# Performance work log

Measured on AMD Instinct MI355X. Metric: run time of the kernel, lower is better.

## Reference

```python
import jax, jax.numpy as jnp
from jax import lax
import numpy as np

K = 10            # size_feat
N_MU = 10         # number of mean-PSF components
NCH = K * K + N_MU  # 110 depthwise channels
KLEN = 65         # precomputed kernel length


def setup_inputs() -> dict:
    key = jax.random.key(0)
    ks = jax.random.split(key, 12)
    B, C, H, W = 1, 3, 256, 256
    img = jax.random.uniform(ks[0], (B, C, H, W), jnp.float32)
    zernike = jax.random.normal(ks[1], (B, H, W, 35), jnp.float32)
    # pos displacements (first 2 channels) scaled to a few pixels
    zernike = zernike.at[..., :2].multiply(2.0)
    fc1_w = jax.random.normal(ks[2], (200, 33), jnp.float32) / np.float32(np.sqrt(33))
    fc1_b = jax.random.normal(ks[3], (200,), jnp.float32) * 0.01
    fc2_w = jax.random.normal(ks[4], (200, 200), jnp.float32) / np.float32(np.sqrt(200))
    fc2_b = jax.random.normal(ks[5], (200,), jnp.float32) * 0.01
    fc3_w = jax.random.normal(ks[6], (100, 200), jnp.float32) * 0.01
    fc3_b = jnp.zeros((100,), jnp.float32)
    basis_left = jax.random.normal(ks[7], (KLEN, K), jnp.float32) * 0.05
    basis_right = jax.random.normal(ks[8], (KLEN, K), jnp.float32) * 0.05
    mu = jax.random.uniform(ks[9], (KLEN, N_MU), jnp.float32) / np.float32(KLEN)
    return dict(img=img, zernike=zernike, fc1_w=fc1_w, fc1_b=fc1_b,
                fc2_w=fc2_w, fc2_b=fc2_b, fc3_w=fc3_w, fc3_b=fc3_b,
                basis_left=basis_left, basis_right=basis_right, mu=mu, ksize=65)


def _grid_sample_border(img, pos):
    """Bilinear grid_sample, padding_mode='border', align_corners=False.
    img: (B,C,H,W), pos: (B,H,W,2) pixel displacements (x,y)."""
    B, C, H, W = img.shape
    yy, xx = jnp.meshgrid(jnp.arange(H, dtype=jnp.float32),
                          jnp.arange(W, dtype=jnp.float32), indexing='ij')
    grid = jnp.stack((xx, yy), -1)                       # (H,W,2)
    wh = jnp.array([W - 1, H - 1], jnp.float32)
    flow = 2.0 * (grid[None] + pos) / wh - 1.0           # (B,H,W,2) in [-1,1]
    ix = ((flow[..., 0] + 1.0) * W - 1.0) * 0.5
    iy = ((flow[..., 1] + 1.0) * H - 1.0) * 0.5
    ix = jnp.clip(ix, 0.0, W - 1)
    iy = jnp.clip(iy, 0.0, H - 1)
    x0 = jnp.floor(ix); y0 = jnp.floor(iy)
    wx = ix - x0;       wy = iy - y0
    x0i = jnp.clip(x0.astype(jnp.int32), 0, W - 1)
    y0i = jnp.clip(y0.astype(jnp.int32), 0, H - 1)
    x1i = jnp.clip(x0i + 1, 0, W - 1)
    y1i = jnp.clip(y0i + 1, 0, H - 1)

    def bilerp(im, x0i, x1i, y0i, y1i, wx, wy):
        g = lambda yi, xi: im[:, yi, xi]                 # (C,H,W)
        top = g(y0i, x0i) * (1 - wx) + g(y0i, x1i) * wx
        bot = g(y1i, x0i) * (1 - wx) + g(y1i, x1i) * wx
        return top * (1 - wy) + bot * wy

    return jax.vmap(bilerp)(img, x0i, x1i, y0i, y1i, wx, wy)


def _depthwise(x, w, pad_axis, pad):
    # x: (N, NCH, H, W); w: (NCH,1,kh,kw). Reflect 'same' padding on pad_axis.
    cfg = [(0, 0)] * 4
    cfg[pad_axis] = (pad, pad)
    xp = jnp.pad(x, cfg, mode='reflect')
    return lax.conv_general_dilated(
        xp, w, (1, 1), 'VALID',
        dimension_numbers=('NCHW', 'OIHW', 'NCHW'),
        feature_group_count=x.shape[1])


def _forward(img, zernike, fc1_w, fc1_b, fc2_w, fc2_b, fc3_w, fc3_b,
             basis_left, basis_right, mu, ksize):
    B, C, H, W = img.shape
    pad = ksize // 2
    # --- grid-sample warp ---
    tilt = _grid_sample_border(img, zernike[..., :2])    # (B,C,H,W)
    # --- per-pixel MLP -> PSF coefficients ---
    f = zernike[..., 2:]                                  # (B,H,W,33)
    h = jax.nn.leaky_relu(f @ fc1_w.T + fc1_b)
    h = jax.nn.leaky_relu(h @ fc2_w.T + fc2_b)
    coef = h @ fc3_w.T + fc3_b                            # (B,H,W,100)
    weight = jnp.concatenate(
        [coef, jnp.ones((B, H, W, N_MU), coef.dtype)], -1)  # (B,H,W,110)
    # --- elementwise weight multiply ---
    big = jnp.concatenate([tilt, jnp.ones_like(tilt)], 1)  # (B,2C,H,W)
    big = big[..., None] * weight[:, None]                 # (B,2C,H,W,110)
    x = big.reshape(B * 2 * C, H, W, NCH).transpose(0, 3, 1, 2)  # (B*2C,110,H,W)
    # --- separable depthwise blur kernels (outer products Z_i x X_j + mu) ---
    wl = jnp.concatenate([jnp.repeat(basis_left.T, K, axis=0), mu.T], 0)  # (110,klen)
    wr = jnp.concatenate([jnp.tile(basis_right.T, (K, 1)), mu.T], 0)      # (110,klen)
    wl = wl[:, None, :, None]                              # (110,1,klen,1)
    wr = wr[:, None, None, :]                              # (110,1,1,klen)
    y = _depthwise(x, wl, 2, pad)
    y = _depthwise(y, wr, 3, pad)
    d = y.reshape(B, 2 * C, NCH, H, W)
    out = jnp.sum(d[:, :3], axis=2) / jnp.sum(d[:, 3:], axis=2)  # (B,3,H,W)
    return out


def reference(img, zernike, fc1_w, fc1_b, fc2_w, fc2_b, fc3_w, fc3_b,
              basis_left, basis_right, mu, ksize):
    return _forward(img, zernike, fc1_w, fc1_b, fc2_w, fc2_b, fc3_w, fc3_b,
                    basis_left, basis_right, mu, ksize)
```

## Files before the change

kernel.cpp:

```cpp
#include <hip/hip_runtime.h>

#define HW 65536

typedef __attribute__((ext_vector_type(8))) short short8;
typedef __attribute__((ext_vector_type(4))) float float4v;

__device__ __forceinline__ int refl(int i){ if (i < 0) i = -i; if (i > 255) i = 510 - i; return i; }
__device__ __forceinline__ float lrelu(float x){ return x > 0.f ? x : 0.01f * x; }
__device__ __forceinline__ unsigned int f2bf(float x){
  union { float f; unsigned int u; } v; v.f = x;
  unsigned int r = v.u + 0x7fff + ((v.u >> 16) & 1);
  return r >> 16;
}
__device__ __forceinline__ unsigned int pk_bf16(float lo, float hi){
  unsigned int r;
  asm("v_cvt_pk_bf16_f32 %0, %1, %2" : "=v"(r) : "v"(lo), "v"(hi));
  return r;
}
__device__ __forceinline__ unsigned short f2h(float x){
  union { _Float16 h; unsigned short u; } v; v.h = (_Float16)x; return v.u;
}
__device__ __forceinline__ float h2f(unsigned short u){
  union { _Float16 h; unsigned short u; } v; v.u = u; return (float)v.h;
}

#define W2OFF 13312
#define W3OFF 59904
__global__ __launch_bounds__(256) void k_prep(const float* __restrict__ img,
    const float* __restrict__ zern,
    const float* __restrict__ w1, const float* __restrict__ w2,
    const float* __restrict__ w3, const float* __restrict__ bl,
    const float* __restrict__ br, const float* __restrict__ mu,
    unsigned short* __restrict__ wbf, unsigned short* __restrict__ Tt,
    float* __restrict__ mucp, float* __restrict__ tilt){
  __shared__ float sm[650];
  __shared__ float sq[10];
  int bid = blockIdx.x;
  int tid = threadIdx.x;
  if (bid < 512){
    int i = bid * 256 + tid;
    if (i < 84992){
      if (i < 208 * 64){
        int n = i >> 6, k = i & 63;
        float v = (n < 200 && k < 33) ? w1[n * 33 + k] : 0.f;
        wbf[i] = (unsigned short)f2bf(v);
      } else if (i < W2OFF + 208 * 224){
        int j = i - W2OFF; int n = j / 224, k = j - n * 224;
        float v = (n < 200 && k < 200) ? w2[n * 200 + k] : 0.f;
        wbf[i] = (unsigned short)f2bf(v);
      } else {
        int j = i - W3OFF; int n = j / 224, k = j - n * 224;
        float v = (n < 100 && k < 200) ? w3[n * 200 + k] : 0.f;
        wbf[i] = (unsigned short)f2bf(v);
      }
    } else {
      int e = i - 84992;
      int t = e / 1536, rem = e - t * 1536;
      int m = rem / 96, k = rem - m * 96;
      int d = k - m;
      float v = 0.f;
      if (d >= 0 && d <= 64){
        if (t < 10)      v = bl[d * 10 + t];
        else if (t < 20) v = mu[d * 10 + (t - 10)];
        else             v = br[d * 10 + (t - 20)];
      }
      Tt[e] = (unsigned short)f2bf(v);
    }
  } else if (bid == 512){
    for (int e = tid; e < 650; e += 256) sm[e] = mu[e];
    __syncthreads();
    if (tid < 10){
      float s = 0.f;
      for (int u = 0; u < 65; ++u) s += sm[u * 10 + tid];
      sq[tid] = s * s;
    }
    __syncthreads();
    if (tid == 0){
      float m = 0.f;
      #pragma unroll
      for (int mm = 0; mm < 10; ++mm) m += sq[mm];
      mucp[0] = m;
    }
  } else {
    int x = tid, y = bid - 513;
    int pix = y * 256 + x;
    float px = zern[pix * 35 + 0], py = zern[pix * 35 + 1];
    float ix = ((float)x + px) * (256.f / 255.f) - 0.5f;
    float iy = ((float)y + py) * (256.f / 255.f) - 0.5f;
    ix = fminf(fmaxf(ix, 0.f), 255.f);
    iy = fminf(fmaxf(iy, 0.f), 255.f);
    float x0f = floorf(ix), y0f = floorf(iy);
    float wx = ix - x0f, wy = iy - y0f;
    int x0 = (int)x0f, y0 = (int)y0f;
    int x1 = min(x0 + 1, 255), y1 = min(y0 + 1, 255);
    #pragma unroll
    for (int c = 0; c < 3; ++c){
      const float* im = img + c * HW;
      float g00 = im[y0 * 256 + x0], g01 = im[y0 * 256 + x1];
      float g10 = im[y1 * 256 + x0], g11 = im[y1 * 256 + x1];
      float top = g00 * (1.f - wx) + g01 * wx;
      float bot = g10 * (1.f - wx) + g11 * wx;
      tilt[c * HW + pix] = top * (1.f - wy) + bot * wy;
    }
  }
}

#define HSTR 232
#define BUFB 14848
__global__ __launch_bounds__(512) void k_mlp(const float* __restrict__ zern,
    const float* __restrict__ b1f, const float* __restrict__ b2f,
    const float* __restrict__ b3f, const unsigned short* __restrict__ wbf,
    unsigned short* __restrict__ coefb){
  __shared__ char smem[2 * BUFB];
  unsigned short* H1  = (unsigned short*)smem;
  unsigned short* XB  = (unsigned short*)(smem + BUFB);
  unsigned short* H2  = XB;
  int tid = threadIdx.x;
  int pix0 = blockIdx.x * 32;
  int lane = tid & 63, wv = tid >> 6;
  int ln = lane & 15, qd = lane >> 4;

  for (int e = tid; e < 1152; e += 512) ((int*)XB)[e] = 0;
  for (int e = tid; e < 384; e += 512){
    int m = e / 12, j = e - m * 12;
    ((int*)H1)[m * 116 + 104 + j] = 0;
  }
  __syncthreads();
  for (int e = tid; e < 32 * 33; e += 512){
    int m = e / 33, k = e - m * 33;
    XB[m * 72 + k] = (unsigned short)f2bf(zern[(pix0 + m) * 35 + 2 + k]);
  }
  __syncthreads();

  for (int nt = wv; nt < 13; nt += 8){
    int n = nt * 16 + ln;
    short8 b0 = *(const short8*)(wbf + n * 64 + qd * 8);
    short8 b1 = *(const short8*)(wbf + n * 64 + 32 + qd * 8);
    float bv = (n < 200) ? b1f[n] : 0.f;
    #pragma unroll
    for (int mt = 0; mt < 2; ++mt){
      float4v acc = {bv, bv, bv, bv};
      short8 a0 = *(const short8*)(XB + (mt * 16 + ln) * 72 + qd * 8);
      short8 a1 = *(const short8*)(XB + (mt * 16 + ln) * 72 + 32 + qd * 8);
      acc = __builtin_amdgcn_mfma_f32_16x16x32_bf16(a0, b0, acc, 0, 0, 0);
      acc = __builtin_amdgcn_mfma_f32_16x16x32_bf16(a1, b1, acc, 0, 0, 0);
      #pragma unroll
      for (int r = 0; r < 4; ++r)
        H1[(mt * 16 + qd * 4 + r) * HSTR + n] = (unsigned short)f2bf(lrelu(acc[r]));
    }
  }
  __syncthreads();

  for (int e = tid; e < 384; e += 512){
    int m = e / 12, j = e - m * 12;
    ((int*)H2)[m * 116 + 104 + j] = 0;
  }
  {
    const unsigned short* w2p = wbf + W2OFF;
    for (int nt = wv; nt < 13; nt += 8){
      int n = nt * 16 + ln;
      short8 bf[7];
      #pragma unroll
      for (int kc = 0; kc < 7; ++kc)
        bf[kc] = *(const short8*)(w2p + n * 224 + kc * 32 + qd * 8);
      float bv = (n < 200) ? b2f[n] : 0.f;
      #pragma unroll
      for (int mt = 0; mt < 2; ++mt){
        float4v acc = {bv, bv, bv, bv};
        #pragma unroll
        for (int kc = 0; kc < 7; ++kc){
          short8 af = *(const short8*)(H1 + (mt * 16 + ln) * HSTR + kc * 32 + qd * 8);
          acc = __builtin_amdgcn_mfma_f32_16x16x32_bf16(af, bf[kc], acc, 0, 0, 0);
        }
        #pragma unroll
        for (int r = 0; r < 4; ++r)
          H2[(mt * 16 + qd * 4 + r) * HSTR + n] = (unsigned short)f2bf(lrelu(acc[r]));
      }
    }
  }
  __syncthreads();

  {
    const unsigned short* w3p = wbf + W3OFF;
    for (int nt = wv; nt < 7; nt += 8){
      int n = nt * 16 + ln;
      short8 bf[7];
      #pragma unroll
      for (int kc = 0; kc < 7; ++kc)
        bf[kc] = *(const short8*)(w3p + n * 224 + kc * 32 + qd * 8);
      float bv = (n < 100) ? b3f[n] : 0.f;
      #pragma unroll
      for (int mt = 0; mt < 2; ++mt){
        float4v acc = {bv, bv, bv, bv};
        #pragma unroll
        for (int kc = 0; kc < 7; ++kc){
          short8 af = *(const short8*)(H2 + (mt * 16 + ln) * HSTR + kc * 32 + qd * 8);
          acc = __builtin_amdgcn_mfma_f32_16x16x32_bf16(af, bf[kc], acc, 0, 0, 0);
        }
        if (n < 100){
          unsigned int lo = (unsigned int)f2h(acc[0]) | ((unsigned int)f2h(acc[1]) << 16);
          unsigned int hi = (unsigned int)f2h(acc[2]) | ((unsigned int)f2h(acc[3]) << 16);
          uint2 val; val.x = lo; val.y = hi;
          *(uint2*)(coefb + n * HW + pix0 + mt * 16 + qd * 4) = val;
        }
      }
    }
  }
}

#define VB 344
__global__ __launch_bounds__(256) void k_vconv16(const float* __restrict__ tilt,
    const unsigned short* __restrict__ coefb, const unsigned short* __restrict__ Tt,
    unsigned short* __restrict__ sbuf, unsigned short* __restrict__ smu){
  __shared__ __align__(16) unsigned short sxb[2][16 * VB];
  int tid = threadIdx.x;
  int bid = blockIdx.x;
  int lane = tid & 63, wv = tid >> 6;
  int ln = lane & 15, qd = lane >> 4;
  int col = tid & 15, seg = tid >> 4;
  int r0 = seg * 20;

  int goff[20];
  #pragma unroll
  for (int q = 0; q < 20; ++q) goff[q] = refl(r0 + q - 32) * 256 + col;

  for (int e = tid; e < 768; e += 256){
    int b = e / 384, r = e - b * 384;
    int cc = r / 24, rp = r - cc * 24;
    sxb[b][cc * VB + 320 + rp] = 0;
  }

  if (bid < 640){
    int s = bid & 15;
    int cj = bid >> 4;
    int c = cj / 10, j = cj - c * 10;
    int x0 = s * 16;
    float treg[20];
    if (c < 3){
      const float* tc = tilt + c * HW + x0;
      #pragma unroll
      for (int q = 0; q < 20; ++q) treg[q] = tc[goff[q]];
    }
    unsigned short pf[20];
    {
      const unsigned short* cq = coefb + j * HW + x0;
      #pragma unroll
      for (int q = 0; q < 20; ++q) pf[q] = cq[goff[q]];
    }
    float4v acc[4];
    #pragma unroll
    for (int t = 0; t < 4; ++t) acc[t] = (float4v){0.f, 0.f, 0.f, 0.f};
    for (int i = 0; i < 10; ++i){
      int us = i & 1;
      unsigned short* sb = sxb[us];
      if (c < 3){
        #pragma unroll
        for (int q = 0; q < 10; ++q){
          float v0 = h2f(pf[2 * q]) * treg[2 * q];
          float v1 = h2f(pf[2 * q + 1]) * treg[2 * q + 1];
          *(unsigned int*)&sb[col * VB + r0 + 2 * q] = pk_bf16(v0, v1);
        }
      } else {
        #pragma unroll
        for (int q = 0; q < 10; ++q){
          *(unsigned int*)&sb[col * VB + r0 + 2 * q] = pk_bf16(h2f(pf[2 * q]), h2f(pf[2 * q + 1]));
        }
      }
      __syncthreads();
      if (i < 9){
        const unsigned short* cn = coefb + ((i + 1) * 10 + j) * HW + x0;
        #pragma unroll
        for (int q = 0; q < 20; ++q) pf[q] = cn[goff[q]];
      }
      const unsigned short* ta = Tt + i * 1536 + ln * 96 + qd * 8;
      short8 A0 = *(const short8*)(ta);
      short8 A1 = *(const short8*)(ta + 32);
      short8 A2 = *(const short8*)(ta + 64);
      #pragma unroll
      for (int t = 0; t < 4; ++t){
        int yt = wv * 4 + t;
        const unsigned short* bp = sb + ln * VB + yt * 16 + qd * 8;
        short8 B0 = *(const short8*)(bp);
        short8 B1 = *(const short8*)(bp + 32);
        short8 B2 = *(const short8*)(bp + 64);
        acc[t] = __builtin_amdgcn_mfma_f32_16x16x32_bf16(A0, B0, acc[t], 0, 0, 0);
        acc[t] = __builtin_amdgcn_mfma_f32_16x16x32_bf16(A1, B1, acc[t], 0, 0, 0);
        acc[t] = __builtin_amdgcn_mfma_f32_16x16x32_bf16(A2, B2, acc[t], 0, 0, 0);
      }
    }
    unsigned short* S = sbuf + (c * 10 + j) * HW + x0 + ln;
    #pragma unroll
    for (int t = 0; t < 4; ++t){
      int yt = wv * 4 + t;
      #pragma unroll
      for (int r = 0; r < 4; ++r)
        S[(yt * 16 + qd * 4 + r) * 256] = (unsigned short)f2bf(acc[t][r]);
    }
  } else {
    int b2 = bid - 640;
    int c = b2 >> 4, s = b2 & 15;
    int x0 = s * 16;
    const float* tc = tilt + c * HW + x0;
    float tv[20];
    #pragma unroll
    for (int q = 0; q < 20; ++q) tv[q] = tc[goff[q]];
    #pragma unroll
    for (int q = 0; q < 10; ++q){
      *(unsigned int*)&sxb[0][col * VB + r0 + 2 * q] = pk_bf16(tv[2 * q], tv[2 * q + 1]);
    }
    __syncthreads();
    for (int m = 0; m < 10; ++m){
      const unsigned short* ta = Tt + (10 + m) * 1536 + ln * 96 + qd * 8;
      short8 A0 = *(const short8*)(ta);
      short8 A1 = *(const short8*)(ta + 32);
      short8 A2 = *(const short8*)(ta + 64);
      float4v acc[4];
      #pragma unroll
      for (int t = 0; t < 4; ++t) acc[t] = (float4v){0.f, 0.f, 0.f, 0.f};
      #pragma unroll
      for (int t = 0; t < 4; ++t){
        int yt = wv * 4 + t;
        const unsigned short* bp = sxb[0] + ln * VB + yt * 16 + qd * 8;
        short8 B0 = *(const short8*)(bp);
        short8 B1 = *(const short8*)(bp + 32);
        short8 B2 = *(const short8*)(bp + 64);
        acc[t] = __builtin_amdgcn_mfma_f32_16x16x32_bf16(A0, B0, acc[t], 0, 0, 0);
        acc[t] = __builtin_amdgcn_mfma_f32_16x16x32_bf16(A1, B1, acc[t], 0, 0, 0);
        acc[t] = __builtin_amdgcn_mfma_f32_16x16x32_bf16(A2, B2, acc[t], 0, 0, 0);
      }
      unsigned short* S = smu + (c * 10 + m) * HW + x0 + ln;
      #pragma unroll
      for (int t = 0; t < 4; ++t){
        int yt = wv * 4 + t;
        #pragma unroll
        for (int r = 0; r < 4; ++r)
          S[(yt * 16 + qd * 4 + r) * 256] = (unsigned short)f2bf(acc[t][r]);
      }
    }
  }
}

#define HS2 344
__global__ __launch_bounds__(256) void k_hconv9(const unsigned short* __restrict__ sbuf,
    const unsigned short* __restrict__ smu, const unsigned short* __restrict__ Tt,
    float* __restrict__ part){
  __shared__ __align__(16) unsigned short sxb[16 * HS2];
  int tid = threadIdx.x;
  int grp = blockIdx.x >> 4;
  int yt  = blockIdx.x & 15;
  int y0 = yt * 16;
  int lane = tid & 63, wv = tid >> 6;
  int ln = lane & 15, qd = lane >> 4;
  int srow = tid >> 4, scol = tid & 15;
  int isbr = (grp < 8);
  int tgt, h;
  if (isbr){ tgt = grp >> 1; h = grp & 1; }
  else     { int g2 = grp - 8; tgt = g2 >> 1; h = g2 & 1; }
  const unsigned short* base = isbr ? (sbuf + tgt * 10 * HW) : (smu + tgt * 10 * HW);
  int tbase = isbr ? 20 : 10;

  for (int e = tid; e < 384; e += 256){
    int rr = e / 24, cp = e - rr * 24;
    sxb[rr * HS2 + 320 + cp] = 0;
  }

  int gx[20];
  #pragma unroll
  for (int q = 0; q < 20; ++q) gx[q] = refl(scol * 20 - 32 + q);

  float4v acc[4];
  #pragma unroll
  for (int t = 0; t < 4; ++t) acc[t] = (float4v){0.f, 0.f, 0.f, 0.f};

  for (int p = 0; p < 5; ++p){
    int col = h * 5 + p;
    const unsigned short* plane = base + col * HW + (y0 + srow) * 256;
    __syncthreads();
    unsigned short v[20];
    #pragma unroll
    for (int q = 0; q < 20; ++q) v[q] = plane[gx[q]];
    #pragma unroll
    for (int q = 0; q < 10; ++q){
      *(unsigned int*)&sxb[srow * HS2 + scol * 20 + 2 * q] =
          (unsigned int)v[2 * q] | ((unsigned int)v[2 * q + 1] << 16);
    }
    __syncthreads();
    const unsigned short* ta = Tt + (tbase + col) * 1536 + ln * 96 + qd * 8;
    short8 A0 = *(const short8*)(ta);
    short8 A1 = *(const short8*)(ta + 32);
    short8 A2 = *(const short8*)(ta + 64);
    #pragma unroll
    for (int t = 0; t < 4; ++t){
      int wt = wv * 4 + t;
      const unsigned short* bp = sxb + ln * HS2 + wt * 16 + qd * 8;
      short8 B0 = *(const short8*)(bp);
      short8 B1 = *(const short8*)(bp + 32);
      short8 B2 = *(const short8*)(bp + 64);
      acc[t] = __builtin_amdgcn_mfma_f32_16x16x32_bf16(A0, B0, acc[t], 0, 0, 0);
      acc[t] = __builtin_amdgcn_mfma_f32_16x16x32_bf16(A1, B1, acc[t], 0, 0, 0);
      acc[t] = __builtin_amdgcn_mfma_f32_16x16x32_bf16(A2, B2, acc[t], 0, 0, 0);
    }
  }
  #pragma unroll
  for (int t = 0; t < 4; ++t){
    int wt = wv * 4 + t;
    float4 res = {acc[t][0], acc[t][1], acc[t][2], acc[t][3]};
    *(float4*)(part + grp * HW + (y0 + ln) * 256 + wt * 16 + qd * 4) = res;
  }
}

__global__ __launch_bounds__(256) void k_final(const float* __restrict__ part,
                                               const float* __restrict__ mucp,
                                               float* __restrict__ out){
  int pix = blockIdx.x * 256 + threadIdx.x;
  float muC = mucp[0];
  float den = part[6 * HW + pix] + part[7 * HW + pix] + muC;
  float inv = 1.f / den;
  #pragma unroll
  for (int c = 0; c < 3; ++c){
    float num = part[(2 * c) * HW + pix] + part[(2 * c + 1) * HW + pix]
              + part[(8 + 2 * c) * HW + pix] + part[(9 + 2 * c) * HW + pix];
    out[c * HW + pix] = num * inv;
  }
}

extern "C" void kernel_launch(void* const* d_in, const int* in_sizes, int n_in,
                              void* d_out, int out_size, void* d_ws, size_t ws_size,
                              hipStream_t stream) {
  const float* img  = (const float*)d_in[0];
  const float* zern = (const float*)d_in[1];
  const float* w1   = (const float*)d_in[2];
  const float* b1   = (const float*)d_in[3];
  const float* w2   = (const float*)d_in[4];
  const float* b2   = (const float*)d_in[5];
  const float* w3   = (const float*)d_in[6];
  const float* b3   = (const float*)d_in[7];
  const float* bl   = (const float*)d_in[8];
  const float* br   = (const float*)d_in[9];
  const float* mu   = (const float*)d_in[10];
  float* out = (float*)d_out;

  float* w = (float*)d_ws;
  float* tilt = w;
  unsigned short* coefb = (unsigned short*)(w + 3 * HW);
  float* part = w + 3 * HW;
  unsigned short* sbuf = (unsigned short*)(w + 53 * HW);
  unsigned short* smu  = (unsigned short*)(w + 73 * HW);
  unsigned short* wbf  = (unsigned short*)(w + 53 * HW);
  unsigned short* Tt   = (unsigned short*)(w + 88 * HW);
  float* mucp = (float*)(Tt + 46080);

  k_prep<<<769, 256, 0, stream>>>(img, zern, w1, w2, w3, bl, br, mu, wbf, Tt, mucp, tilt);
  k_mlp<<<2048, 512, 0, stream>>>(zern, b1, b2, b3, wbf, coefb);
  k_vconv16<<<688, 256, 0, stream>>>(tilt, coefb, Tt, sbuf, smu);
  k_hconv9<<<224, 256, 0, stream>>>(sbuf, smu, Tt, part);
  k_final<<<256, 256, 0, stream>>>(part, mucp, out);
}
```

Baseline: 149.4 us.

## Store MLP coefficients column-major so vertical conv reads them contiguously

```diff
diff --git a/kernel.cpp b/kernel.cpp
--- a/kernel.cpp
+++ b/kernel.cpp
@@ -116,7 +116,8 @@
   unsigned short* XB  = (unsigned short*)(smem + BUFB);
   unsigned short* H2  = XB;
   int tid = threadIdx.x;
-  int pix0 = blockIdx.x * 32;
+  int xcol = blockIdx.x >> 3;
+  int y0   = (blockIdx.x & 7) * 32;
   int lane = tid & 63, wv = tid >> 6;
   int ln = lane & 15, qd = lane >> 4;
 
@@ -128,7 +129,7 @@
   __syncthreads();
   for (int e = tid; e < 32 * 33; e += 512){
     int m = e / 33, k = e - m * 33;
-    XB[m * 72 + k] = (unsigned short)f2bf(zern[(pix0 + m) * 35 + 2 + k]);
+    XB[m * 72 + k] = (unsigned short)f2bf(zern[(((y0 + m) << 8) + xcol) * 35 + 2 + k]);
   }
   __syncthreads();
 
@@ -201,7 +202,7 @@
           unsigned int lo = (unsigned int)f2h(acc[0]) | ((unsigned int)f2h(acc[1]) << 16);
           unsigned int hi = (unsigned int)f2h(acc[2]) | ((unsigned int)f2h(acc[3]) << 16);
           uint2 val; val.x = lo; val.y = hi;
-          *(uint2*)(coefb + n * HW + pix0 + mt * 16 + qd * 4) = val;
+          *(uint2*)(coefb + n * HW + xcol * 256 + y0 + mt * 16 + qd * 4) = val;
         }
       }
     }
@@ -209,7 +210,7 @@
 }
 
 #define VB 344
-__global__ __launch_bounds__(256) void k_vconv16(const float* __restrict__ tilt,
+__global__ __launch_bounds__(256) void k_vconv19(const float* __restrict__ tilt,
     const unsigned short* __restrict__ coefb, const unsigned short* __restrict__ Tt,
     unsigned short* __restrict__ sbuf, unsigned short* __restrict__ smu){
   __shared__ __align__(16) unsigned short sxb[2][16 * VB];
@@ -219,10 +220,12 @@
   int ln = lane & 15, qd = lane >> 4;
   int col = tid & 15, seg = tid >> 4;
   int r0 = seg * 20;
+  int yb = r0 - 32;
+  int interior = (seg >= 2) && (seg <= 13);
 
   int goff[20];
   #pragma unroll
-  for (int q = 0; q < 20; ++q) goff[q] = refl(r0 + q - 32) * 256 + col;
+  for (int q = 0; q < 20; ++q) goff[q] = refl(yb + q) * 256 + col;
 
   for (int e = tid; e < 768; e += 256){
     int b = e / 384, r = e - b * 384;
@@ -235,17 +238,28 @@
     int cj = bid >> 4;
     int c = cj / 10, j = cj - c * 10;
     int x0 = s * 16;
+    int xc = x0 + col;
     float treg[20];
     if (c < 3){
       const float* tc = tilt + c * HW + x0;
       #pragma unroll
       for (int q = 0; q < 20; ++q) treg[q] = tc[goff[q]];
     }
-    unsigned short pf[20];
+    unsigned int pf32[10];
     {
-      const unsigned short* cq = coefb + j * HW + x0;
-      #pragma unroll
-      for (int q = 0; q < 20; ++q) pf[q] = cq[goff[q]];
+      const unsigned short* cqb = coefb + j * HW + xc * 256;
+      if (interior){
+        const unsigned int* p32 = (const unsigned int*)(cqb + yb);
+        #pragma unroll
+        for (int q = 0; q < 10; ++q) pf32[q] = p32[q];
+      } else {
+        #pragma unroll
+        for (int q = 0; q < 10; ++q){
+          unsigned int lo = cqb[refl(yb + 2 * q)];
+          unsigned int hi = cqb[refl(yb + 2 * q + 1)];
+          pf32[q] = lo | (hi << 16);
+        }
+      }
     }
     float4v acc[4];
     #pragma unroll
@@ -256,21 +270,33 @@
       if (c < 3){
         #pragma unroll
         for (int q = 0; q < 10; ++q){
-          float v0 = h2f(pf[2 * q]) * treg[2 * q];
-          float v1 = h2f(pf[2 * q + 1]) * treg[2 * q + 1];
+          float v0 = h2f((unsigned short)(pf32[q] & 0xffff)) * treg[2 * q];
+          float v1 = h2f((unsigned short)(pf32[q] >> 16))    * treg[2 * q + 1];
           *(unsigned int*)&sb[col * VB + r0 + 2 * q] = pk_bf16(v0, v1);
         }
       } else {
         #pragma unroll
         for (int q = 0; q < 10; ++q){
-          *(unsigned int*)&sb[col * VB + r0 + 2 * q] = pk_bf16(h2f(pf[2 * q]), h2f(pf[2 * q + 1]));
+          float v0 = h2f((unsigned short)(pf32[q] & 0xffff));
+          float v1 = h2f((unsigned short)(pf32[q] >> 16));
+          *(unsigned int*)&sb[col * VB + r0 + 2 * q] = pk_bf16(v0, v1);
         }
       }
       __syncthreads();
       if (i < 9){
-        const unsigned short* cn = coefb + ((i + 1) * 10 + j) * HW + x0;
-        #pragma unroll
-        for (int q = 0; q < 20; ++q) pf[q] = cn[goff[q]];
+        const unsigned short* cnb = coefb + ((i + 1) * 10 + j) * HW + xc * 256;
+        if (interior){
+          const unsigned int* p32 = (const unsigned int*)(cnb + yb);
+          #pragma unroll
+          for (int q = 0; q < 10; ++q) pf32[q] = p32[q];
+        } else {
+          #pragma unroll
+          for (int q = 0; q < 10; ++q){
+            unsigned int lo = cnb[refl(yb + 2 * q)];
+            unsigned int hi = cnb[refl(yb + 2 * q + 1)];
+            pf32[q] = lo | (hi << 16);
+          }
+        }
       }
       const unsigned short* ta = Tt + i * 1536 + ln * 96 + qd * 8;
       short8 A0 = *(const short8*)(ta);
@@ -452,7 +478,7 @@
 
   k_prep<<<769, 256, 0, stream>>>(img, zern, w1, w2, w3, bl, br, mu, wbf, Tt, mucp, tilt);
   k_mlp<<<2048, 512, 0, stream>>>(zern, b1, b2, b3, wbf, coefb);
-  k_vconv16<<<688, 256, 0, stream>>>(tilt, coefb, Tt, sbuf, smu);
+  k_vconv19<<<688, 256, 0, stream>>>(tilt, coefb, Tt, sbuf, smu);
   k_hconv9<<<224, 256, 0, stream>>>(sbuf, smu, Tt, part);
   k_final<<<256, 256, 0, stream>>>(part, mucp, out);
 }
```

After: 167.5 us. 1.12x slower.
